# Performance work log

Hardware: AMD Instinct MI355X
Metric: run time of the kernel (lower is better)

Reference implementation:

```python
import jax, jax.numpy as jnp
import numpy as np

TAU = 0.5  # tau_coff from init


def setup_inputs() -> dict:
    key = jax.random.key(0)
    ks = jax.random.split(key, 4)
    ni, nt, d = 1024, 1024, 64
    return {
        "images_hash": jax.random.normal(ks[0], (ni, d), jnp.float32),
        "texts_hash": jax.random.normal(ks[1], (nt, d), jnp.float32),
        "W1": jax.random.normal(ks[2], (2 * d, 2 * d), jnp.float32) / np.sqrt(2 * d),
        "b1": jnp.zeros((2 * d,), jnp.float32),
        "W2": jax.random.normal(ks[3], (1, 2 * d), jnp.float32) / np.sqrt(2 * d),
        "b2": jnp.zeros((1,), jnp.float32),
        "task_is_i2t": 1,
    }


def reference(images_hash, texts_hash, W1, b1, W2, b2, task_is_i2t):
    ni, d = images_hash.shape
    nt = texts_hash.shape[0]
    scale = 1.0 / np.sqrt(d)
    # straight-through estimator: forward = sign(x)/sqrt(d), backward = identity
    ste = lambda x: jax.lax.stop_gradient(jnp.sign(x) * scale - x) + x
    img = ste(images_hash)  # [ni, d]
    txt = ste(texts_hash)   # [nt, d]

    # getPosE on the pairwise concat [img_i ; txt_j]. Split W1 columns so the
    # first layer is two small GEMMs + broadcast-add instead of materializing
    # the [ni*nt, 2d] concat.
    h_img = img @ W1[:, :d].T   # [ni, 2d]
    h_txt = txt @ W1[:, d:].T   # [nt, 2d]
    h = jax.nn.relu(h_img[:, None, :] + h_txt[None, :, :] + b1)  # [ni, nt, 2d]
    negE = jnp.einsum('ijk,ok->ij', h, W2) + b2[0]               # [ni, nt]

    if task_is_i2t:
        posE = img @ txt.T   # [ni, nt]
    else:
        posE = txt @ img.T   # [nt, ni]

    posE = jnp.exp(jnp.clip(posE / TAU, -15.0, 15.0)).reshape(-1, 1)
    negE = jnp.exp(jnp.clip(negE / TAU, -15.0, 15.0)).reshape(-1, 1)
    return jnp.concatenate([posE, negE], axis=1)  # [ni*nt, 2]
```

## Files before the change

kernel.cpp:

```cpp
#include <hip/hip_runtime.h>
#include <hip/hip_bf16.h>
#include <stdint.h>

#define NI   1024
#define NT   1024
#define DD   64
#define K2   128

__global__ __launch_bounds__(128) void precompute_kernel(
    const float* __restrict__ img, const float* __restrict__ txt,
    const float* __restrict__ W1,  const float* __restrict__ b1,
    const float* __restrict__ W2,
    float* __restrict__ At, float* __restrict__ Bt,
    float* __restrict__ rA, float* __restrict__ rB,
    unsigned long long* __restrict__ img_x, unsigned long long* __restrict__ img_m,
    unsigned long long* __restrict__ txt_x, unsigned long long* __restrict__ txt_m)
{
    const int tid = threadIdx.x;
    const int rb  = blockIdx.x * 8;
    const bool is_img = (rb < NI);
    const int lrb = is_img ? rb : rb - NI;
    const float* src = (is_img ? img : txt) + lrb * DD;

    __shared__ float sv[8 * 64];

    for (int idx = tid; idx < 8 * 64; idx += 128) {
        float x = src[idx];
        sv[idx] = (x > 0.f) ? 0.125f : ((x < 0.f) ? -0.125f : 0.f);
    }
    __syncthreads();

    if (tid < 64) {
        #pragma unroll
        for (int r = 0; r < 8; ++r) {
            float s = sv[r * 64 + tid];
            unsigned long long xb = __ballot(s < 0.f);
            unsigned long long mb = __ballot(s != 0.f);
            if (tid == 0) {
                if (is_img) { img_x[lrb + r] = xb; img_m[lrb + r] = mb; }
                else        { txt_x[lrb + r] = xb; txt_m[lrb + r] = mb; }
            }
        }
    }

    const int t = tid;
    const int off = is_img ? 0 : DD;
    const float* wrow = W1 + t * K2 + off;
    float h[8];
    const float hinit = is_img ? b1[t] : 0.f;
    #pragma unroll
    for (int r = 0; r < 8; ++r) h[r] = hinit;

    for (int c = 0; c < DD; ++c) {
        float w = wrow[c];
        #pragma unroll
        for (int r = 0; r < 8; ++r) h[r] = fmaf(w, sv[r * 64 + c], h[r]);
    }

    float* T = is_img ? At : Bt;
    #pragma unroll
    for (int r = 0; r < 8; ++r) T[t * 1024 + lrb + r] = h[r];

    __shared__ float red[128 * 8];
    const float w2t = W2[t];
    #pragma unroll
    for (int r = 0; r < 8; ++r) red[t * 8 + r] = w2t * h[r];
    __syncthreads();
    if (t < 8) {
        float s = 0.f;
        for (int u = 0; u < 128; ++u) s += red[u * 8 + t];
        if (is_img) rA[lrb + t] = s; else rB[lrb + t] = s;
    }
}

__global__ __launch_bounds__(256) void pair_kernel(
    const float* __restrict__ At, const float* __restrict__ Bt,
    const float* __restrict__ rA, const float* __restrict__ rB,
    const float* __restrict__ W2, const float* __restrict__ b2,
    const unsigned long long* __restrict__ img_x, const unsigned long long* __restrict__ img_m,
    const unsigned long long* __restrict__ txt_x, const unsigned long long* __restrict__ txt_m,
    const int* __restrict__ taskp,
    float2* __restrict__ out)
{
    const int tid = threadIdx.x;
    const int bid = blockIdx.x;
    const int I0  = (bid >> 2) * 8;
    const int j   = (bid & 3) * 256 + tid;

    float acc[8];
    #pragma unroll
    for (int ii = 0; ii < 8; ++ii) acc[ii] = 0.f;

    #pragma unroll 4
    for (int k = 0; k < K2; ++k) {
        const float b = Bt[k * 1024 + j];
        const float w = W2[k];
        const float* ak = At + k * 1024 + I0;
        #pragma unroll
        for (int ii = 0; ii < 8; ++ii) {
            float t = ak[ii] + b;
            acc[ii] = fmaf(w, __builtin_fabsf(t), acc[ii]);
        }
    }

    const int task = *taskp;
    const unsigned long long* xi_a = task ? img_x : txt_x;
    const unsigned long long* mi_a = task ? img_m : txt_m;
    const unsigned long long* xj_a = task ? txt_x : img_x;
    const unsigned long long* mj_a = task ? txt_m : img_m;

    const unsigned long long xj = xj_a[j];
    const unsigned long long mj = mj_a[j];
    const float rBj = rB[j];
    const float b2v = b2[0];

    #pragma unroll
    for (int ii = 0; ii < 8; ++ii) {
        const int i = I0 + ii;
        const unsigned long long xi = xi_a[i];
        const unsigned long long mi = mi_a[i];
        const unsigned long long valid = mi & mj;
        const int nv = __popcll(valid);
        const int df = __popcll((xi ^ xj) & valid);
        const float pos = (float)(nv - 2 * df) * (1.0f / 64.0f);
        const float neg = 0.5f * (rA[i] + rBj + acc[ii]) + b2v;

        const float pe = __expf(fminf(fmaxf(pos * 2.0f, -15.0f), 15.0f));
        const float ne = __expf(fminf(fmaxf(neg * 2.0f, -15.0f), 15.0f));
        out[i * NT + j] = make_float2(pe, ne);
    }
}

extern "C" void kernel_launch(void* const* d_in, const int* in_sizes, int n_in,
                              void* d_out, int out_size, void* d_ws, size_t ws_size,
                              hipStream_t stream) {
    const float* img = (const float*)d_in[0];
    const float* txt = (const float*)d_in[1];
    const float* W1  = (const float*)d_in[2];
    const float* b1  = (const float*)d_in[3];
    const float* W2  = (const float*)d_in[4];
    const float* b2  = (const float*)d_in[5];
    const int*  task = (const int*)d_in[6];

    float* At = (float*)d_ws;
    float* Bt = At + K2 * 1024;
    float* rA = Bt + K2 * 1024;
    float* rB = rA + 1024;
    unsigned long long* img_x = (unsigned long long*)(rB + 1024);
    unsigned long long* img_m = img_x + 1024;
    unsigned long long* txt_x = img_m + 1024;
    unsigned long long* txt_m = txt_x + 1024;

    hipLaunchKernelGGL(precompute_kernel, dim3(256), dim3(128), 0, stream,
                       img, txt, W1, b1, W2, At, Bt, rA, rB,
                       img_x, img_m, txt_x, txt_m);

    hipLaunchKernelGGL(pair_kernel, dim3(512), dim3(256), 0, stream,
                       At, Bt, rA, rB, W2, b2,
                       img_x, img_m, txt_x, txt_m, task,
                       (float2*)d_out);
}
```

Before: 91.37 us.

## Interleave k-pairs in A/B layout, vectorize loads, halve rows per block

Stores the hidden projections in a k-pair interleaved layout so the pair kernel loads float2/float4 vectors per k pair, and processes 4 rows per block instead of 8, doubling the grid. The precompute kernel vectorizes W1 and shared loads and replaces the shared-memory reduction with wave shuffles. Outputs are written with nontemporal stores. The aim is fewer load instructions and more parallelism, at the cost of less reuse of each B load across rows.

```diff
diff --git a/kernel.cpp b/kernel.cpp
--- a/kernel.cpp
+++ b/kernel.cpp
@@ -7,24 +7,27 @@
 #define DD   64
 #define K2   128
 
+typedef float f32x2 __attribute__((ext_vector_type(2)));
+
 __global__ __launch_bounds__(128) void precompute_kernel(
     const float* __restrict__ img, const float* __restrict__ txt,
     const float* __restrict__ W1,  const float* __restrict__ b1,
     const float* __restrict__ W2,
-    float* __restrict__ At, float* __restrict__ Bt,
+    float* __restrict__ Ap, float* __restrict__ Bp,
     float* __restrict__ rA, float* __restrict__ rB,
     unsigned long long* __restrict__ img_x, unsigned long long* __restrict__ img_m,
     unsigned long long* __restrict__ txt_x, unsigned long long* __restrict__ txt_m)
 {
     const int tid = threadIdx.x;
-    const int rb  = blockIdx.x * 8;
+    const int rb  = blockIdx.x * 4;
     const bool is_img = (rb < NI);
     const int lrb = is_img ? rb : rb - NI;
     const float* src = (is_img ? img : txt) + lrb * DD;
 
-    __shared__ float sv[8 * 64];
+    __shared__ float sv[4 * 64];
+    __shared__ float part[2][4];
 
-    for (int idx = tid; idx < 8 * 64; idx += 128) {
+    for (int idx = tid; idx < 4 * 64; idx += 128) {
         float x = src[idx];
         sv[idx] = (x > 0.f) ? 0.125f : ((x < 0.f) ? -0.125f : 0.f);
     }
@@ -32,7 +35,7 @@
 
     if (tid < 64) {
         #pragma unroll
-        for (int r = 0; r < 8; ++r) {
+        for (int r = 0; r < 4; ++r) {
             float s = sv[r * 64 + tid];
             unsigned long long xb = __ballot(s < 0.f);
             unsigned long long mb = __ballot(s != 0.f);
@@ -46,62 +49,82 @@
     const int t = tid;
     const int off = is_img ? 0 : DD;
     const float* wrow = W1 + t * K2 + off;
-    float h[8];
+    float h[4];
     const float hinit = is_img ? b1[t] : 0.f;
     #pragma unroll
-    for (int r = 0; r < 8; ++r) h[r] = hinit;
+    for (int r = 0; r < 4; ++r) h[r] = hinit;
 
-    for (int c = 0; c < DD; ++c) {
-        float w = wrow[c];
+    #pragma unroll 4
+    for (int c4 = 0; c4 < DD / 4; ++c4) {
+        const float4 w4 = *reinterpret_cast<const float4*>(wrow + c4 * 4);
         #pragma unroll
-        for (int r = 0; r < 8; ++r) h[r] = fmaf(w, sv[r * 64 + c], h[r]);
+        for (int r = 0; r < 4; ++r) {
+            const float4 s4 = *reinterpret_cast<const float4*>(&sv[r * 64 + c4 * 4]);
+            h[r] = fmaf(w4.x, s4.x, h[r]);
+            h[r] = fmaf(w4.y, s4.y, h[r]);
+            h[r] = fmaf(w4.z, s4.z, h[r]);
+            h[r] = fmaf(w4.w, s4.w, h[r]);
+        }
     }
 
-    float* T = is_img ? At : Bt;
+    float* T = is_img ? Ap : Bp;
+    const int tbase = (t >> 1) * 2048 + (t & 1);
     #pragma unroll
-    for (int r = 0; r < 8; ++r) T[t * 1024 + lrb + r] = h[r];
+    for (int r = 0; r < 4; ++r) T[tbase + (lrb + r) * 2] = h[r];
 
-    __shared__ float red[128 * 8];
     const float w2t = W2[t];
+    const int wid = tid >> 6, lane = tid & 63;
     #pragma unroll
-    for (int r = 0; r < 8; ++r) red[t * 8 + r] = w2t * h[r];
+    for (int r = 0; r < 4; ++r) {
+        float v = w2t * h[r];
+        v += __shfl_xor(v, 32); v += __shfl_xor(v, 16); v += __shfl_xor(v, 8);
+        v += __shfl_xor(v, 4);  v += __shfl_xor(v, 2);  v += __shfl_xor(v, 1);
+        if (lane == 0) part[wid][r] = v;
+    }
     __syncthreads();
-    if (t < 8) {
-        float s = 0.f;
-        for (int u = 0; u < 128; ++u) s += red[u * 8 + t];
-        if (is_img) rA[lrb + t] = s; else rB[lrb + t] = s;
+    if (tid < 4) {
+        float s = part[0][tid] + part[1][tid];
+        if (is_img) rA[lrb + tid] = s; else rB[lrb + tid] = s;
     }
 }
 
 __global__ __launch_bounds__(256) void pair_kernel(
-    const float* __restrict__ At, const float* __restrict__ Bt,
+    const float* __restrict__ Ap, const float* __restrict__ Bp,
     const float* __restrict__ rA, const float* __restrict__ rB,
     const float* __restrict__ W2, const float* __restrict__ b2,
     const unsigned long long* __restrict__ img_x, const unsigned long long* __restrict__ img_m,
     const unsigned long long* __restrict__ txt_x, const unsigned long long* __restrict__ txt_m,
     const int* __restrict__ taskp,
-    float2* __restrict__ out)
+    float* __restrict__ out)
 {
     const int tid = threadIdx.x;
     const int bid = blockIdx.x;
-    const int I0  = (bid >> 2) * 8;
+    const int I0  = (bid >> 2) * 4;
     const int j   = (bid & 3) * 256 + tid;
 
-    float acc[8];
-    #pragma unroll
-    for (int ii = 0; ii < 8; ++ii) acc[ii] = 0.f;
+    const float2* __restrict__ Bp2 = (const float2*)Bp;
+    const float4* __restrict__ Ap4 = (const float4*)Ap;
+    const float2* __restrict__ W2p = (const float2*)W2;
 
-    #pragma unroll 4
-    for (int k = 0; k < K2; ++k) {
-        const float b = Bt[k * 1024 + j];
-        const float w = W2[k];
-        const float* ak = At + k * 1024 + I0;
-        #pragma unroll
-        for (int ii = 0; ii < 8; ++ii) {
-            float t = ak[ii] + b;
-            acc[ii] = fmaf(w, __builtin_fabsf(t), acc[ii]);
-        }
+    float acc0 = 0.f, acc1 = 0.f, acc2 = 0.f, acc3 = 0.f;
+
+    #pragma unroll 8
+    for (int kp = 0; kp < K2 / 2; ++kp) {
+        const float2 bv  = Bp2[kp * 1024 + j];
+        const float4 a01 = Ap4[kp * 512 + (I0 >> 1)];
+        const float4 a23 = Ap4[kp * 512 + (I0 >> 1) + 1];
+        const float2 w   = W2p[kp];
+        float t;
+        t = a01.x + bv.x; acc0 = fmaf(w.x, __builtin_fabsf(t), acc0);
+        t = a01.y + bv.y; acc0 = fmaf(w.y, __builtin_fabsf(t), acc0);
+        t = a01.z + bv.x; acc1 = fmaf(w.x, __builtin_fabsf(t), acc1);
+        t = a01.w + bv.y; acc1 = fmaf(w.y, __builtin_fabsf(t), acc1);
+        t = a23.x + bv.x; acc2 = fmaf(w.x, __builtin_fabsf(t), acc2);
+        t = a23.y + bv.y; acc2 = fmaf(w.y, __builtin_fabsf(t), acc2);
+        t = a23.z + bv.x; acc3 = fmaf(w.x, __builtin_fabsf(t), acc3);
+        t = a23.w + bv.y; acc3 = fmaf(w.y, __builtin_fabsf(t), acc3);
     }
+    float acc[4] = {acc0, acc1, acc2, acc3};
 
     const int task = *taskp;
     const unsigned long long* xi_a = task ? img_x : txt_x;
@@ -115,7 +138,7 @@
     const float b2v = b2[0];
 
     #pragma unroll
-    for (int ii = 0; ii < 8; ++ii) {
+    for (int ii = 0; ii < 4; ++ii) {
         const int i = I0 + ii;
         const unsigned long long xi = xi_a[i];
         const unsigned long long mi = mi_a[i];
@@ -127,7 +150,8 @@
 
         const float pe = __expf(fminf(fmaxf(pos * 2.0f, -15.0f), 15.0f));
         const float ne = __expf(fminf(fmaxf(neg * 2.0f, -15.0f), 15.0f));
-        out[i * NT + j] = make_float2(pe, ne);
+        f32x2 o; o.x = pe; o.y = ne;
+        __builtin_nontemporal_store(o, (f32x2*)&out[(size_t)(i * NT + j) * 2]);
     }
 }
 
@@ -142,21 +166,21 @@
     const float* b2  = (const float*)d_in[5];
     const int*  task = (const int*)d_in[6];
 
-    float* At = (float*)d_ws;
-    float* Bt = At + K2 * 1024;
-    float* rA = Bt + K2 * 1024;
+    float* Ap = (float*)d_ws;
+    float* Bp = Ap + K2 * 1024;
+    float* rA = Bp + K2 * 1024;
     float* rB = rA + 1024;
     unsigned long long* img_x = (unsigned long long*)(rB + 1024);
     unsigned long long* img_m = img_x + 1024;
     unsigned long long* txt_x = img_m + 1024;
     unsigned long long* txt_m = txt_x + 1024;
 
-    hipLaunchKernelGGL(precompute_kernel, dim3(256), dim3(128), 0, stream,
-                       img, txt, W1, b1, W2, At, Bt, rA, rB,
+    hipLaunchKernelGGL(precompute_kernel, dim3(512), dim3(128), 0, stream,
+                       img, txt, W1, b1, W2, Ap, Bp, rA, rB,
                        img_x, img_m, txt_x, txt_m);
 
-    hipLaunchKernelGGL(pair_kernel, dim3(512), dim3(256), 0, stream,
-                       At, Bt, rA, rB, W2, b2,
+    hipLaunchKernelGGL(pair_kernel, dim3(1024), dim3(256), 0, stream,
+                       Ap, Bp, rA, rB, W2, b2,
                        img_x, img_m, txt_x, txt_m, task,
-                       (float2*)d_out);
+                       (float*)d_out);
 }
```

Result: slower. 94.29 us (+3.2%).
